# Kernel tuning notes

Measured on AMD Instinct MI355X. Metric: run time of the kernel, lower is better.

The kernel has to match this reference:

```python
import jax, jax.numpy as jnp
import numpy as np

B, I, H = 16384, 512, 512


def setup_inputs() -> dict:
    key = jax.random.key(0)
    ks = jax.random.split(key, 9)
    std = 1.0 / np.sqrt(H)
    u = lambda k, shape: jax.random.uniform(k, shape, jnp.float32, -std, std)
    return {
        "input": jax.random.normal(ks[0], (B, I), jnp.float32),
        "h_prev": jax.random.normal(ks[1], (B, H), jnp.float32),
        "c_prev": jax.random.normal(ks[2], (B, H), jnp.float32),
        "m_prev": jax.random.normal(ks[3], (B, H), jnp.float32),
        "n_prev": jnp.ones((B, H), jnp.float32),
        "Wxh": u(ks[4], (4 * H, I)),
        "bxh": u(ks[5], (4 * H,)),
        "Whh": u(ks[6], (4 * H, H)),
        "bhh": u(ks[7], (4 * H,)),
    }


def reference(input, h_prev, c_prev, m_prev, n_prev, Wxh, bxh, Whh, bhh):
    # gates = xh(input) + hh(h_prev) -> [B, 4H]
    gates = input @ Wxh.T + bxh + h_prev @ Whh.T + bhh
    ig, fg, zg, og = jnp.split(gates, 4, axis=1)
    z_t = jnp.tanh(zg)
    o_t = jax.nn.sigmoid(og)
    # log-space stabilizer: log(exp(fg)) = fg, log(exp(ig)) = ig
    m_t = jnp.maximum(fg + m_prev, ig)
    i_t = jnp.exp(ig - m_t)
    f_t = jnp.exp(fg + m_prev - m_t)
    c_t = f_t * c_prev + i_t * z_t
    n_t = f_t * n_prev + i_t
    h_t = o_t * (c_t / n_t)
    return (h_t, c_t, m_t, n_t)
```

## Files before the change

### kernel.cpp

```cpp
#include <hip/hip_runtime.h>

#define Bsz 16384
#define Isz 512
#define Hsz 512
#define Ksz 1024
#define N4H 2048

#define BM 256
#define BN 256
#define BK 64

typedef __bf16 bf16x8 __attribute__((ext_vector_type(8)));
typedef __bf16 bf16x4 __attribute__((ext_vector_type(4)));
typedef float  f32x4  __attribute__((ext_vector_type(4)));

__device__ __forceinline__ void async_copy16(const void* g, void* l) {
    __builtin_amdgcn_global_load_lds(
        (__attribute__((address_space(1))) void*)g,
        (__attribute__((address_space(3))) void*)l,
        16, 0, 0);
}

__global__ void pack_all(const float* __restrict__ x, const float* __restrict__ h,
                         const float* __restrict__ Wxh, const float* __restrict__ Whh,
                         const float* __restrict__ bxh, const float* __restrict__ bhh,
                         __bf16* __restrict__ Aq, __bf16* __restrict__ Bq,
                         float* __restrict__ bias) {
    if (blockIdx.x < 16384) {
        int idx = blockIdx.x * 256 + threadIdx.x;
        int e   = idx << 2;
        int row = e >> 10, col = e & 1023;
        const float4 v = (col < Isz)
            ? *(const float4*)(x + (size_t)row * Isz + col)
            : *(const float4*)(h + (size_t)row * Hsz + (col - Isz));
        bf16x4 o = { (__bf16)v.x, (__bf16)v.y, (__bf16)v.z, (__bf16)v.w };
        *(bf16x4*)(Aq + (size_t)e) = o;
    } else {
        int idx = (blockIdx.x - 16384) * 256 + threadIdx.x;
        int p   = idx >> 8;
        int k   = (idx & 255) << 2;
        int nb  = p >> 7, n = p & 127;
        int wn  = n >> 6, t = (n >> 4) & 3, c = n & 15;
        int orow = t * Hsz + nb * 32 + wn * 16 + c;
        const float4 v = (k < Isz)
            ? *(const float4*)(Wxh + (size_t)orow * Isz + k)
            : *(const float4*)(Whh + (size_t)orow * Hsz + (k - Isz));
        bf16x4 o = { (__bf16)v.x, (__bf16)v.y, (__bf16)v.z, (__bf16)v.w };
        *(bf16x4*)(Bq + (size_t)p * Ksz + k) = o;
        if ((idx & 255) == 0) bias[p] = bxh[orow] + bhh[orow];
    }
}

#define CFENCE asm volatile("" ::: "memory")
#define BARRIER { CFENCE; __builtin_amdgcn_s_barrier(); CFENCE; }
#define WAITLGKM asm volatile("s_waitcnt lgkmcnt(0)" ::: "memory")
#define WAITVM4  asm volatile("s_waitcnt vmcnt(4)" ::: "memory")

#define LDS_A(ap, fbase)                                                      \
    _Pragma("unroll") for (int f = 0; f < 4; ++f)                             \
    _Pragma("unroll") for (int kk = 0; kk < 2; ++kk)                          \
        af[f][kk] = *(const bf16x8*)((ap) + (fbase + f) * 1024 + ko[kk]);

#define LDS_B(bp, nbase)                                                      \
    _Pragma("unroll") for (int n = 0; n < 2; ++n)                             \
    _Pragma("unroll") for (int kk = 0; kk < 2; ++kk)                          \
        bf[(nbase) + n][kk] = *(const bf16x8*)((bp) + ((nbase) + n) * 1024 + ko[kk]);

#define MMA(fbase, nbase)                                                     \
    __builtin_amdgcn_s_setprio(1);                                            \
    _Pragma("unroll") for (int f = 0; f < 4; ++f)                             \
    _Pragma("unroll") for (int n = 0; n < 2; ++n)                             \
    _Pragma("unroll") for (int kk = 0; kk < 2; ++kk)                          \
        acc[(fbase) + f][(nbase) + n] = __builtin_amdgcn_mfma_f32_16x16x32_bf16( \
            af[f][kk], bf[(nbase) + n][kk], acc[(fbase) + f][(nbase) + n], 0, 0, 0); \
    __builtin_amdgcn_s_setprio(0);

#define STAGE(arr, buf, half, src, step)                                      \
    { async_copy16((src) + (size_t)((half) * 128 + rrow) * Ksz + (step) * 64 + scol, \
                   (char*)(arr) + (buf) * 32768 + (half) * 16384 + tid * 16); \
      async_copy16((src) + (size_t)((half) * 128 + 64 + rrow) * Ksz + (step) * 64 + scol, \
                   (char*)(arr) + (buf) * 32768 + (half) * 16384 + 8192 + tid * 16); }

__global__ __launch_bounds__(512, 2) void slstm_gemm(
    const __bf16* __restrict__ Aq, const __bf16* __restrict__ Bq,
    const float* __restrict__ bias,
    const float* __restrict__ c_prev, const float* __restrict__ m_prev,
    const float* __restrict__ n_prev, float* __restrict__ out) {

    __shared__ __bf16 As[2][BM * BK];
    __shared__ __bf16 Bs[2][BN * BK];

    const int tid  = threadIdx.x;
    const int w    = tid >> 6;
    const int lane = tid & 63;
    const int wm   = w & 1;
    const int wc   = w >> 1;

    const int pid = blockIdx.x;
    const int xcd = pid & 7;
    const int jj  = (pid >> 3) & 31;
    const int rr  = pid >> 8;
    const int bm  = xcd * 8 + (jj & 3) + rr * 4;
    const int nbb = jj >> 2;

    const int lr = lane & 15;
    const int g0 = lane >> 4;
    const int px = lr & 7;

    const __bf16* Ag = Aq + (size_t)bm  * BM * Ksz;
    const __bf16* Bg = Bq + (size_t)nbb * BN * Ksz;

    const int rrow = tid >> 3;
    const int scol = ((tid & 7) ^ (rrow & 7)) * 8;

    const __bf16* A0p = &As[0][(wm * 128 + lr) * 64];
    const __bf16* A1p = &As[1][(wm * 128 + lr) * 64];
    const __bf16* B0p = &Bs[0][(wc * 64 + lr) * 64];
    const __bf16* B1p = &Bs[1][(wc * 64 + lr) * 64];
    const int ko[2] = { ((0 * 4 + g0) ^ px) * 8, ((1 * 4 + g0) ^ px) * 8 };

    __bf16* AsB = &As[0][0];
    __bf16* BsB = &Bs[0][0];

    f32x4 acc[8][4];
    const f32x4 zero = {0.f, 0.f, 0.f, 0.f};
#pragma unroll
    for (int mi = 0; mi < 8; ++mi)
#pragma unroll
        for (int ni = 0; ni < 4; ++ni) acc[mi][ni] = zero;

    STAGE(BsB, 0, 0, Bg, 0);
    STAGE(BsB, 0, 1, Bg, 0);
    STAGE(AsB, 0, 0, Ag, 0);
    STAGE(AsB, 0, 1, Ag, 0);
    STAGE(BsB, 1, 0, Bg, 1);
    STAGE(BsB, 1, 1, Bg, 1);
    WAITVM4;
    BARRIER;

    bf16x8 af[4][2];
    bf16x8 bf[4][2];

#pragma unroll 1
    for (int i = 0; i < 8; ++i) {
        const int ic  = (i < 7) ? i : 6;
        const int sA1 = 2 * i + 1;
        const int sB0 = 2 * ic + 2;
        const int sB1 = 2 * ic + 3;

        LDS_A(A0p, 0);
        LDS_B(B0p, 0);
        STAGE(AsB, 1, 0, Ag, sA1);
        BARRIER; WAITLGKM;
        MMA(0, 0);
        BARRIER;

        LDS_B(B0p, 2);
        STAGE(AsB, 1, 1, Ag, sA1);
        BARRIER; WAITLGKM;
        MMA(0, 2);
        BARRIER;

        LDS_A(A0p, 4);
        STAGE(BsB, 0, 0, Bg, sB0);
        BARRIER; WAITLGKM;
        MMA(4, 2);
        BARRIER;

        STAGE(BsB, 0, 1, Bg, sB0);
        BARRIER;
        MMA(4, 0);
        WAITVM4;
        BARRIER;

        LDS_A(A1p, 0);
        LDS_B(B1p, 0);
        STAGE(AsB, 0, 0, Ag, sB0);
        BARRIER; WAITLGKM;
        MMA(0, 0);
        BARRIER;

        LDS_B(B1p, 2);
        STAGE(AsB, 0, 1, Ag, sB0);
        BARRIER; WAITLGKM;
        MMA(0, 2);
        BARRIER;

        LDS_A(A1p, 4);
        STAGE(BsB, 1, 0, Bg, sB1);
        BARRIER; WAITLGKM;
        MMA(4, 2);
        BARRIER;

        STAGE(BsB, 1, 1, Bg, sB1);
        BARRIER;
        MMA(4, 0);
        WAITVM4;
        BARRIER;
    }

    const int hidx = (nbb * 2 + (wc >> 1)) * 32 + (wc & 1) * 16 + lr;

    float bsv[4];
#pragma unroll
    for (int n = 0; n < 4; ++n)
        bsv[n] = bias[nbb * 256 + wc * 64 + n * 16 + lr];

    const size_t BH = (size_t)Bsz * Hsz;

#pragma unroll
    for (int mi = 0; mi < 8; ++mi) {
        const int mbase = bm * 256 + wm * 128 + mi * 16 + g0 * 4;
#pragma unroll
        for (int r = 0; r < 4; ++r) {
            const int m = mbase + r;
            const size_t off = (size_t)m * Hsz + hidx;
            const float ig = acc[mi][0][r] + bsv[0];
            const float fg = acc[mi][1][r] + bsv[1];
            const float zg = acc[mi][2][r] + bsv[2];
            const float og = acc[mi][3][r] + bsv[3];
            const float cp = c_prev[off];
            const float mp = m_prev[off];
            const float np = n_prev[off];
            const float zt = tanhf(zg);
            const float ot = 1.f / (1.f + expf(-og));
            const float fm = fg + mp;
            const float mt = fmaxf(fm, ig);
            const float it = expf(ig - mt);
            const float ft = expf(fm - mt);
            const float ct = ft * cp + it * zt;
            const float nt = ft * np + it;
            const float ht = ot * (ct / nt);
            out[off]          = ht;
            out[BH + off]     = ct;
            out[2 * BH + off] = mt;
            out[3 * BH + off] = nt;
        }
    }
}

extern "C" void kernel_launch(void* const* d_in, const int* in_sizes, int n_in,
                              void* d_out, int out_size, void* d_ws, size_t ws_size,
                              hipStream_t stream) {
    const float* input  = (const float*)d_in[0];
    const float* h_prev = (const float*)d_in[1];
    const float* c_prev = (const float*)d_in[2];
    const float* m_prev = (const float*)d_in[3];
    const float* n_prev = (const float*)d_in[4];
    const float* Wxh    = (const float*)d_in[5];
    const float* bxh    = (const float*)d_in[6];
    const float* Whh    = (const float*)d_in[7];
    const float* bhh    = (const float*)d_in[8];
    float* out = (float*)d_out;

    __bf16* Aq   = (__bf16*)d_ws;
    __bf16* Bq   = (__bf16*)((char*)d_ws + (size_t)Bsz * Ksz * 2);
    float*  bias = (float*)((char*)d_ws + (size_t)Bsz * Ksz * 2 + (size_t)N4H * Ksz * 2);

    pack_all<<<16384 + 2048, 256, 0, stream>>>(input, h_prev, Wxh, Whh, bxh, bhh,
                                               Aq, Bq, bias);

    slstm_gemm<<<512, 512, 0, stream>>>(Aq, Bq, bias, c_prev, m_prev, n_prev, out);
}
```

Baseline: 356.8 us.

## Use inline-asm LDS reads with immediate offsets, split LDS buffers, simplify block mapping

```diff
diff --git a/kernel.cpp b/kernel.cpp
--- a/kernel.cpp
+++ b/kernel.cpp
@@ -53,18 +53,32 @@
 
 #define CFENCE asm volatile("" ::: "memory")
 #define BARRIER { CFENCE; __builtin_amdgcn_s_barrier(); CFENCE; }
-#define WAITLGKM asm volatile("s_waitcnt lgkmcnt(0)" ::: "memory")
+#define WAITLGKM { asm volatile("s_waitcnt lgkmcnt(0)" ::: "memory"); \
+                   __builtin_amdgcn_sched_barrier(0); }
 #define WAITVM4  asm volatile("s_waitcnt vmcnt(4)" ::: "memory")
 
-#define LDS_A(ap, fbase)                                                      \
-    _Pragma("unroll") for (int f = 0; f < 4; ++f)                             \
-    _Pragma("unroll") for (int kk = 0; kk < 2; ++kk)                          \
-        af[f][kk] = *(const bf16x8*)((ap) + (fbase + f) * 1024 + ko[kk]);
-
-#define LDS_B(bp, nbase)                                                      \
-    _Pragma("unroll") for (int n = 0; n < 2; ++n)                             \
-    _Pragma("unroll") for (int kk = 0; kk < 2; ++kk)                          \
-        bf[(nbase) + n][kk] = *(const bf16x8*)((bp) + ((nbase) + n) * 1024 + ko[kk]);
+#define LDSA(p) ((unsigned)(size_t)(const __bf16 __attribute__((address_space(3)))*)(p))
+
+#define DSR(dst, addr, IMM) \
+    asm volatile("ds_read_b128 %0, %1 offset:" IMM : "=v"(dst) : "v"(addr))
+
+#define LDS_A_(ap, I0, I1, I2, I3) { \
+    const unsigned a0_ = LDSA((ap) + ko0), a1_ = LDSA((ap) + ko1); \
+    DSR(af[0][0], a0_, I0); DSR(af[0][1], a1_, I0); \
+    DSR(af[1][0], a0_, I1); DSR(af[1][1], a1_, I1); \
+    DSR(af[2][0], a0_, I2); DSR(af[2][1], a1_, I2); \
+    DSR(af[3][0], a0_, I3); DSR(af[3][1], a1_, I3); }
+#define LDS_A0(ap) LDS_A_(ap, "0", "2048", "4096", "6144")
+#define LDS_A4(ap) LDS_A_(ap, "8192", "10240", "12288", "14336")
+
+#define LDS_B0(bp) { \
+    const unsigned b0_ = LDSA((bp) + ko0), b1_ = LDSA((bp) + ko1); \
+    DSR(bf[0][0], b0_, "0");    DSR(bf[0][1], b1_, "0"); \
+    DSR(bf[1][0], b0_, "2048"); DSR(bf[1][1], b1_, "2048"); }
+#define LDS_B2(bp) { \
+    const unsigned b0_ = LDSA((bp) + ko0), b1_ = LDSA((bp) + ko1); \
+    DSR(bf[2][0], b0_, "4096"); DSR(bf[2][1], b1_, "4096"); \
+    DSR(bf[3][0], b0_, "6144"); DSR(bf[3][1], b1_, "6144"); }
 
 #define MMA(fbase, nbase)                                                     \
     __builtin_amdgcn_s_setprio(1);                                            \
@@ -75,11 +89,11 @@
             af[f][kk], bf[(nbase) + n][kk], acc[(fbase) + f][(nbase) + n], 0, 0, 0); \
     __builtin_amdgcn_s_setprio(0);
 
-#define STAGE(arr, buf, half, src, step)                                      \
+#define STAGE(dst, src, half, step)                                           \
     { async_copy16((src) + (size_t)((half) * 128 + rrow) * Ksz + (step) * 64 + scol, \
-                   (char*)(arr) + (buf) * 32768 + (half) * 16384 + tid * 16); \
+                   (char*)(dst) + (half) * 16384 + tid * 16);                 \
       async_copy16((src) + (size_t)((half) * 128 + 64 + rrow) * Ksz + (step) * 64 + scol, \
-                   (char*)(arr) + (buf) * 32768 + (half) * 16384 + 8192 + tid * 16); }
+                   (char*)(dst) + (half) * 16384 + 8192 + tid * 16); }
 
 __global__ __launch_bounds__(512, 2) void slstm_gemm(
     const __bf16* __restrict__ Aq, const __bf16* __restrict__ Bq,
@@ -87,8 +101,10 @@
     const float* __restrict__ c_prev, const float* __restrict__ m_prev,
     const float* __restrict__ n_prev, float* __restrict__ out) {
 
-    __shared__ __bf16 As[2][BM * BK];
-    __shared__ __bf16 Bs[2][BN * BK];
+    __shared__ __bf16 As0[BM * BK];
+    __shared__ __bf16 As1[BM * BK];
+    __shared__ __bf16 Bs0[BN * BK];
+    __shared__ __bf16 Bs1[BN * BK];
 
     const int tid  = threadIdx.x;
     const int w    = tid >> 6;
@@ -97,11 +113,8 @@
     const int wc   = w >> 1;
 
     const int pid = blockIdx.x;
-    const int xcd = pid & 7;
-    const int jj  = (pid >> 3) & 31;
-    const int rr  = pid >> 8;
-    const int bm  = xcd * 8 + (jj & 3) + rr * 4;
-    const int nbb = jj >> 2;
+    const int bm  = pid >> 3;
+    const int nbb = pid & 7;
 
     const int lr = lane & 15;
     const int g0 = lane >> 4;
@@ -113,14 +126,12 @@
     const int rrow = tid >> 3;
     const int scol = ((tid & 7) ^ (rrow & 7)) * 8;
 
-    const __bf16* A0p = &As[0][(wm * 128 + lr) * 64];
-    const __bf16* A1p = &As[1][(wm * 128 + lr) * 64];
-    const __bf16* B0p = &Bs[0][(wc * 64 + lr) * 64];
-    const __bf16* B1p = &Bs[1][(wc * 64 + lr) * 64];
-    const int ko[2] = { ((0 * 4 + g0) ^ px) * 8, ((1 * 4 + g0) ^ px) * 8 };
-
-    __bf16* AsB = &As[0][0];
-    __bf16* BsB = &Bs[0][0];
+    const __bf16* A0p = &As0[(wm * 128 + lr) * 64];
+    const __bf16* A1p = &As1[(wm * 128 + lr) * 64];
+    const __bf16* B0p = &Bs0[(wc * 64 + lr) * 64];
+    const __bf16* B1p = &Bs1[(wc * 64 + lr) * 64];
+    const int ko0 = ((0 * 4 + g0) ^ px) * 8;
+    const int ko1 = ((1 * 4 + g0) ^ px) * 8;
 
     f32x4 acc[8][4];
     const f32x4 zero = {0.f, 0.f, 0.f, 0.f};
@@ -129,12 +140,12 @@
 #pragma unroll
         for (int ni = 0; ni < 4; ++ni) acc[mi][ni] = zero;
 
-    STAGE(BsB, 0, 0, Bg, 0);
-    STAGE(BsB, 0, 1, Bg, 0);
-    STAGE(AsB, 0, 0, Ag, 0);
-    STAGE(AsB, 0, 1, Ag, 0);
-    STAGE(BsB, 1, 0, Bg, 1);
-    STAGE(BsB, 1, 1, Bg, 1);
+    STAGE(Bs0, Bg, 0, 0);
+    STAGE(Bs0, Bg, 1, 0);
+    STAGE(As0, Ag, 0, 0);
+    STAGE(As0, Ag, 1, 0);
+    STAGE(Bs1, Bg, 0, 1);
+    STAGE(Bs1, Bg, 1, 1);
     WAITVM4;
     BARRIER;
 
@@ -148,51 +159,51 @@
         const int sB0 = 2 * ic + 2;
         const int sB1 = 2 * ic + 3;
 
-        LDS_A(A0p, 0);
-        LDS_B(B0p, 0);
-        STAGE(AsB, 1, 0, Ag, sA1);
+        LDS_A0(A0p);
+        LDS_B0(B0p);
+        STAGE(As1, Ag, 0, sA1);
         BARRIER; WAITLGKM;
         MMA(0, 0);
         BARRIER;
 
-        LDS_B(B0p, 2);
-        STAGE(AsB, 1, 1, Ag, sA1);
+        LDS_B2(B0p);
+        STAGE(As1, Ag, 1, sA1);
         BARRIER; WAITLGKM;
         MMA(0, 2);
         BARRIER;
 
-        LDS_A(A0p, 4);
-        STAGE(BsB, 0, 0, Bg, sB0);
+        LDS_A4(A0p);
+        STAGE(Bs0, Bg, 0, sB0);
         BARRIER; WAITLGKM;
         MMA(4, 2);
         BARRIER;
 
-        STAGE(BsB, 0, 1, Bg, sB0);
+        STAGE(Bs0, Bg, 1, sB0);
         BARRIER;
         MMA(4, 0);
         WAITVM4;
         BARRIER;
 
-        LDS_A(A1p, 0);
-        LDS_B(B1p, 0);
-        STAGE(AsB, 0, 0, Ag, sB0);
+        LDS_A0(A1p);
+        LDS_B0(B1p);
+        STAGE(As0, Ag, 0, sB0);
         BARRIER; WAITLGKM;
         MMA(0, 0);
         BARRIER;
 
-        LDS_B(B1p, 2);
-        STAGE(AsB, 0, 1, Ag, sB0);
+        LDS_B2(B1p);
+        STAGE(As0, Ag, 1, sB0);
         BARRIER; WAITLGKM;
         MMA(0, 2);
         BARRIER;
 
-        LDS_A(A1p, 4);
-        STAGE(BsB, 1, 0, Bg, sB1);
+        LDS_A4(A1p);
+        STAGE(Bs1, Bg, 0, sB1);
         BARRIER; WAITLGKM;
         MMA(4, 2);
         BARRIER;
 
-        STAGE(BsB, 1, 1, Bg, sB1);
+        STAGE(Bs1, Bg, 1, sB1);
         BARRIER;
         MMA(4, 0);
         WAITVM4;
```

Measured after the change: 354.9 us. About the same (-0.5%).
